# Performance work log

Measured on AMD Instinct MI355X. Metric: run time of the kernel, lower is better.

## Reference

```python
import jax, jax.numpy as jnp
import numpy as np

N_NODES = 50000
N_EDGES = 800000
NODE_F = 5
EDGE_F = 4
HID = 128


def _glorot(key, shape):
    fan_in, fan_out = shape[0], shape[1]
    lim = float(np.sqrt(6.0 / (fan_in + fan_out)))
    return jax.random.uniform(key, shape, jnp.float32, -lim, lim)


def setup_inputs() -> dict:
    key = jax.random.key(0)
    ks = jax.random.split(key, 12)
    x = jax.random.normal(ks[0], (N_NODES, NODE_F), jnp.float32)
    edge_attr = jax.random.normal(ks[1], (N_EDGES, EDGE_F), jnp.float32)
    edge_index = jax.random.randint(ks[2], (2, N_EDGES), 0, N_NODES, jnp.int64)
    return {
        "x": x,
        "edge_attr": edge_attr,
        "W1": _glorot(ks[3], (NODE_F, HID)),
        "b1": jnp.zeros((HID,), jnp.float32),
        "W2": _glorot(ks[4], (HID, HID)),
        "b2": jnp.zeros((HID,), jnp.float32),
        "Wm1": _glorot(ks[5], (2 * HID + EDGE_F, HID)),
        "bm1": jnp.zeros((HID,), jnp.float32),
        "Wm2": _glorot(ks[6], (HID, 1)),
        "bm2": jnp.zeros((1,), jnp.float32),
        "edge_index": edge_index,
    }


def _gcn_conv(x, W, b, row, col, norm, n_nodes):
    # GCNConv: out = D^{-1/2} (A + I) D^{-1/2} X W + b
    xw = x @ W                                   # [N, H]
    msg = norm[:, None] * xw[row]                # [E+N, H] gather + scale
    agg = jax.ops.segment_sum(msg, col, num_segments=n_nodes)
    return agg + b


def reference(x, edge_attr, W1, b1, W2, b2, Wm1, bm1, Wm2, bm2, edge_index):
    n = x.shape[0]
    src, dst = edge_index[0], edge_index[1]
    # add self-loops (PyG GCNConv default)
    loop = jnp.arange(n, dtype=edge_index.dtype)
    row = jnp.concatenate([src, loop])
    col = jnp.concatenate([dst, loop])
    # symmetric normalization, in-degree w/ self-loops
    deg = jax.ops.segment_sum(jnp.ones_like(col, dtype=x.dtype), col, num_segments=n)
    dis = jnp.where(deg > 0, jax.lax.rsqrt(deg), 0.0)
    norm = dis[row] * dis[col]

    h = jax.nn.relu(_gcn_conv(x, W1, b1, row, col, norm, n))
    h = _gcn_conv(h, W2, b2, row, col, norm, n)

    # gather-concat edge MLP
    edge_emb = jnp.concatenate([h[src], h[dst], edge_attr], axis=1)  # [E, 2H+F]
    out = jax.nn.relu(edge_emb @ Wm1 + bm1) @ Wm2 + bm2              # [E, 1]
    return jax.nn.sigmoid(out[:, 0])
```

## Files before the change

### kernel.cpp

```cpp
#include <hip/hip_runtime.h>
#include <math.h>

#define HID 128
typedef unsigned int uint;
typedef __attribute__((ext_vector_type(8))) __bf16 bf16x8;
typedef __attribute__((ext_vector_type(4))) float f32x4;
typedef __attribute__((ext_vector_type(2))) float f32x2;


__device__ __forceinline__ uint pack_bf2(float x, float y) {
    union { float f; uint u; } a, b;
    a.f = x; b.f = y;
    uint lo = (a.u + 0x7fffu + ((a.u >> 16) & 1u)) >> 16;
    uint hi = (b.u + 0x7fffu + ((b.u >> 16) & 1u)) & 0xffff0000u;
    return lo | hi;
}

__device__ __forceinline__ unsigned short bf16r(float x) {
    union { float f; uint u; } a; a.f = x;
    return (unsigned short)((a.u + 0x7fffu + ((a.u >> 16) & 1u)) >> 16);
}

__device__ __forceinline__ f32x2 bf2f(uint v) {
    union { uint u[2]; f32x2 f; } r;
    r.u[0] = v << 16;
    r.u[1] = v & 0xffff0000u;
    return r.f;
}

__device__ __forceinline__ f32x2 mk2(float s) { f32x2 r; r.x = s; r.y = s; return r; }
__device__ __forceinline__ f32x2 max2z(f32x2 a) {
    f32x2 r; r.x = fmaxf(a.x, 0.f); r.y = fmaxf(a.y, 0.f); return r;
}
__device__ __forceinline__ f32x2 shfl_xor2(f32x2 v, int m) {
    f32x2 r; r.x = __shfl_xor(v.x, m, 64); r.y = __shfl_xor(v.y, m, 64); return r;
}


__global__ void prep_kernel(const float* __restrict__ W2, const float* __restrict__ Wm1,
                            const float* __restrict__ b2, const float* __restrict__ bm1,
                            uint* __restrict__ fWc, float* __restrict__ brow) {
    int t0 = blockIdx.x * blockDim.x + threadIdx.x;
    if (t0 < 16384) {
        int i = t0;
        int p = i & 3, lane = (i >> 2) & 63, kk = (i >> 8) & 3, ct = i >> 10;
        int k = kk * 32 + (lane >> 4) * 8 + p * 2;
        int n2 = ct * 16 + (lane & 15);
        const float* wmc = (n2 < 128) ? (Wm1 + n2) : (Wm1 + 128 * HID + (n2 - 128));
        const float* w2r0 = W2 + (size_t)k * HID;
        const float* w2r1 = w2r0 + HID;
        float d0 = 0.f, d1 = 0.f;
        for (int j = 0; j < HID; ++j) {
            float wm = wmc[(size_t)j * HID];
            d0 += w2r0[j] * wm;
            d1 += w2r1[j] * wm;
        }
        fWc[i] = pack_bf2(d0, d1);
    } else if (t0 < 16384 + 256) {
        int i = t0 - 16384;
        const float* wmc = (i < 128) ? (Wm1 + i) : (Wm1 + 128 * HID + (i - 128));
        float d = 0.f;
        for (int j = 0; j < HID; ++j) d += b2[j] * wmc[(size_t)j * HID];
        brow[i] = d + ((i < 128) ? bm1[i] : 0.f);
    }
}

__global__ void hist_rank(const int* __restrict__ dst, int* __restrict__ cnt,
                          int* __restrict__ rank, int E) {
    int e = blockIdx.x * blockDim.x + threadIdx.x;
    if (e < E) rank[e] = atomicAdd(&cnt[dst[e]], 1);
}

__global__ void scan1(const int* __restrict__ cnt, int* __restrict__ excl,
                      int* __restrict__ bsum, int N) {
    __shared__ int sh[256];
    int tid = threadIdx.x;
    int gid = blockIdx.x * 256 + tid;
    int v = (gid < N) ? cnt[gid] : 0;
    sh[tid] = v;
    __syncthreads();
    for (int o = 1; o < 256; o <<= 1) {
        int t = (tid >= o) ? sh[tid - o] : 0;
        __syncthreads();
        sh[tid] += t;
        __syncthreads();
    }
    if (gid < N) excl[gid] = sh[tid] - v;
    if (tid == 255) bsum[blockIdx.x] = sh[255];
}

__global__ void scan3x(const int* __restrict__ cnt, int* __restrict__ rowptr,
                       const int* __restrict__ bsum,
                       float* __restrict__ dis, const float* __restrict__ x,
                       uint4* __restrict__ xps, int N, int E, int NB) {
    __shared__ int sh[256];
    __shared__ int ex[256];
    int tid = threadIdx.x;
    int v = (tid < NB) ? bsum[tid] : 0;
    sh[tid] = v;
    __syncthreads();
    for (int o = 1; o < 256; o <<= 1) {
        int t = (tid >= o) ? sh[tid - o] : 0;
        __syncthreads();
        sh[tid] += t;
        __syncthreads();
    }
    ex[tid] = sh[tid] - v;
    __syncthreads();
    int gid = blockIdx.x * 256 + tid;
    if (gid < N) {
        rowptr[gid] = rowptr[gid] + ex[blockIdx.x];
        float dn = rsqrtf((float)cnt[gid] + 1.0f);
        dis[gid] = dn;
        const float* xr = x + (size_t)gid * 5;
        uint4 pk;
        pk.x = pack_bf2(dn * xr[0], dn * xr[1]);
        pk.y = pack_bf2(dn * xr[2], dn * xr[3]);
        pk.z = pack_bf2(dn * xr[4], 0.f);
        pk.w = 0u;
        xps[gid] = pk;
    }
    if (gid == N) rowptr[N] = E;
}

__global__ void scatter2(const int* __restrict__ src, const int* __restrict__ dst,
                         const int* __restrict__ rowptr, const int* __restrict__ rank,
                         uint2* __restrict__ csr2, int E) {
    int e = blockIdx.x * blockDim.x + threadIdx.x;
    if (e < E) {
        int d = dst[e];
        int pos = rowptr[d] + rank[e];
        csr2[pos] = make_uint2((uint)src[e] | ((uint)d << 16), (uint)e);
    }
}

__launch_bounds__(256)
__global__ void layer1_kernel(const uint4* __restrict__ xps, const uint2* __restrict__ csr2,
                              const int* __restrict__ rowptr, const float* __restrict__ dis,
                              const float* __restrict__ W1, const float* __restrict__ b1,
                              uint* __restrict__ hs1, int N) {
    __shared__ float sW[5 * HID];
    __shared__ float sb[HID];
    int tid = threadIdx.x;
    for (int i = tid; i < 5 * HID; i += 256) sW[i] = W1[i];
    for (int i = tid; i < HID; i += 256) sb[i] = b1[i];
    __syncthreads();

    int n = blockIdx.x * 256 + tid;
    if (n >= N) return;
    int beg = rowptr[n], end = rowptr[n + 1];
    float a0 = 0.f, a1 = 0.f, a2 = 0.f, a3 = 0.f, a4 = 0.f;
    for (int i = beg; i < end; ++i) {
        int s = (int)(csr2[i].x & 0xffffu);
        uint4 v = xps[s];
        f32x2 v01 = bf2f(v.x), v23 = bf2f(v.y), v4 = bf2f(v.z);
        a0 += v01.x; a1 += v01.y; a2 += v23.x; a3 += v23.y; a4 += v4.x;
    }
    {
        uint4 v = xps[n];
        f32x2 v01 = bf2f(v.x), v23 = bf2f(v.y), v4 = bf2f(v.z);
        a0 += v01.x; a1 += v01.y; a2 += v23.x; a3 += v23.y; a4 += v4.x;
    }
    float dn = dis[n];
    a0 *= dn; a1 *= dn; a2 *= dn; a3 *= dn; a4 *= dn;

    uint* op = hs1 + (size_t)n * 64;
    #pragma unroll 4
    for (int p = 0; p < 64; ++p) {
        int j = p * 2;
        float t0 = sb[j]     + a0 * sW[j]     + a1 * sW[HID + j]     + a2 * sW[2*HID + j]
                             + a3 * sW[3*HID + j] + a4 * sW[4*HID + j];
        float t1 = sb[j + 1] + a0 * sW[j + 1] + a1 * sW[HID + j + 1] + a2 * sW[2*HID + j + 1]
                             + a3 * sW[3*HID + j + 1] + a4 * sW[4*HID + j + 1];
        op[p] = pack_bf2(fmaxf(t0, 0.f) * dn, fmaxf(t1, 0.f) * dn);
    }
}

__launch_bounds__(256)
__global__ void agg_gemm(const uint4* __restrict__ hs1, const uint2* __restrict__ csr2,
                         const int* __restrict__ rowptr, const float* __restrict__ dis,
                         const uint4* __restrict__ Bf, const float* __restrict__ brow,
                         unsigned short* __restrict__ out, int N) {
    __shared__ uint gt[16][64];
    int wave = threadIdx.x >> 6, lane = threadIdx.x & 63;
    int gl = lane & 15, grp = lane >> 4;
    int nb = blockIdx.x * 16;

    for (int q = 0; q < 4; ++q) {
        int r = wave * 4 + q;
        int n = nb + r;
        if (n < N) {
            int beg = rowptr[n], end = rowptr[n + 1];
            f32x2 acc[4];
            #pragma unroll
            for (int p = 0; p < 4; ++p) acc[p] = mk2(0.f);
            for (int base = beg + grp; base < end; base += 16) {
                int i1 = base + 4, i2 = base + 8, i3 = base + 12;
                int s0 = (int)(csr2[base].x & 0xffffu);
                int s1 = (int)(csr2[(i1 < end) ? i1 : beg].x & 0xffffu);
                int s2 = (int)(csr2[(i2 < end) ? i2 : beg].x & 0xffffu);
                int s3 = (int)(csr2[(i3 < end) ? i3 : beg].x & 0xffffu);
                uint4 v0 = hs1[(size_t)s0 * 16 + gl];
                uint4 v1 = hs1[(size_t)s1 * 16 + gl];
                uint4 v2 = hs1[(size_t)s2 * 16 + gl];
                uint4 v3 = hs1[(size_t)s3 * 16 + gl];
                f32x2 w1 = mk2((i1 < end) ? 1.f : 0.f);
                f32x2 w2 = mk2((i2 < end) ? 1.f : 0.f);
                f32x2 w3 = mk2((i3 < end) ? 1.f : 0.f);
                acc[0] += bf2f(v0.x);  acc[1] += bf2f(v0.y);
                acc[2] += bf2f(v0.z);  acc[3] += bf2f(v0.w);
                acc[0] += bf2f(v1.x) * w1;  acc[1] += bf2f(v1.y) * w1;
                acc[2] += bf2f(v1.z) * w1;  acc[3] += bf2f(v1.w) * w1;
                acc[0] += bf2f(v2.x) * w2;  acc[1] += bf2f(v2.y) * w2;
                acc[2] += bf2f(v2.z) * w2;  acc[3] += bf2f(v2.w) * w2;
                acc[0] += bf2f(v3.x) * w3;  acc[1] += bf2f(v3.y) * w3;
                acc[2] += bf2f(v3.z) * w3;  acc[3] += bf2f(v3.w) * w3;
            }
            #pragma unroll
            for (int p = 0; p < 4; ++p) {
                acc[p] += shfl_xor2(acc[p], 16);
                acc[p] += shfl_xor2(acc[p], 32);
            }
            if (grp == 0) {
                uint4 sv = hs1[(size_t)n * 16 + gl];
                f32x2 dn = mk2(dis[n]);
                f32x2 o0 = (acc[0] + bf2f(sv.x)) * dn;
                f32x2 o1 = (acc[1] + bf2f(sv.y)) * dn;
                f32x2 o2 = (acc[2] + bf2f(sv.z)) * dn;
                f32x2 o3 = (acc[3] + bf2f(sv.w)) * dn;
                gt[r][gl * 4]     = pack_bf2(o0.x, o0.y);
                gt[r][gl * 4 + 1] = pack_bf2(o1.x, o1.y);
                gt[r][gl * 4 + 2] = pack_bf2(o2.x, o2.y);
                gt[r][gl * 4 + 3] = pack_bf2(o3.x, o3.y);
            }
        } else if (grp == 0) {
            gt[r][gl * 4] = 0; gt[r][gl * 4 + 1] = 0;
            gt[r][gl * 4 + 2] = 0; gt[r][gl * 4 + 3] = 0;
        }
    }
    __syncthreads();

    int quad = lane >> 4;
    bf16x8 afr[4];
    #pragma unroll
    for (int kk = 0; kk < 4; ++kk)
        afr[kk] = *(const bf16x8*)&gt[gl][kk * 16 + quad * 4];

    for (int cc = 0; cc < 4; ++cc) {
        int c = wave * 4 + cc;
        f32x4 acc = {0.f, 0.f, 0.f, 0.f};
        #pragma unroll
        for (int kk = 0; kk < 4; ++kk) {
            bf16x8 bfr = *(const bf16x8*)&Bf[(size_t)(c * 4 + kk) * 64 + lane];
            acc = __builtin_amdgcn_mfma_f32_16x16x32_bf16(afr[kk], bfr, acc, 0, 0, 0);
        }
        float bv = brow[c * 16 + gl];
        #pragma unroll
        for (int reg = 0; reg < 4; ++reg) {
            int row = nb + quad * 4 + reg;
            if (row < N)
                out[(size_t)row * 256 + c * 16 + gl] = bf16r(acc[reg] + bv);
        }
    }
}

__launch_bounds__(256)
__global__ void edge_mlp_kernel(const uint4* __restrict__ HsHd, const float4* __restrict__ ea,
                                const uint2* __restrict__ csr2,
                                const float* __restrict__ Wb, const float* __restrict__ Wm2,
                                const float* __restrict__ bm2,
                                float* __restrict__ out, int E) {
    int lane = threadIdx.x & 63;
    int gl = lane & 15, grp = lane >> 4;

    f32x2 wb[4][4], w2[4];
    #pragma unroll
    for (int k = 0; k < 4; ++k) {
        const f32x2* wp = (const f32x2*)(Wb + k * HID + gl * 8);
        #pragma unroll
        for (int p = 0; p < 4; ++p) wb[k][p] = wp[p];
    }
    {
        const f32x2* wp = (const f32x2*)(Wm2 + gl * 8);
        #pragma unroll
        for (int p = 0; p < 4; ++p) w2[p] = wp[p];
    }
    float b2v = bm2[0];

    int gwave = (blockIdx.x * blockDim.x + threadIdx.x) >> 6;
    int nw = (gridDim.x * blockDim.x) >> 6;
    for (int base = gwave * 16; base < E; base += nw * 16) {
        int i0 = base + grp * 4;
        uint2 ce[4];
        uint4 hv[4], dv[4];
        float4 eav[4];
        #pragma unroll
        for (int t = 0; t < 4; ++t) {
            int i = i0 + t;
            int j = (i < E) ? i : (E - 1);
            ce[t] = csr2[j];
            hv[t] = HsHd[(size_t)(ce[t].x & 0xffffu) * 32 + gl];
            dv[t] = HsHd[(size_t)(ce[t].x >> 16) * 32 + 16 + gl];
            eav[t] = ea[ce[t].y];
        }
        float pr[4];
        #pragma unroll
        for (int t = 0; t < 4; ++t) {
            uint hu[4] = {hv[t].x, hv[t].y, hv[t].z, hv[t].w};
            uint du[4] = {dv[t].x, dv[t].y, dv[t].z, dv[t].w};
            f32x2 e0 = mk2(eav[t].x), e1 = mk2(eav[t].y);
            f32x2 e2 = mk2(eav[t].z), e3 = mk2(eav[t].w);
            f32x2 p2 = mk2(0.f);
            #pragma unroll
            for (int p = 0; p < 4; ++p) {
                f32x2 tt = bf2f(hu[p]) + bf2f(du[p]);
                tt += e0 * wb[0][p];
                tt += e1 * wb[1][p];
                tt += e2 * wb[2][p];
                tt += e3 * wb[3][p];
                tt = max2z(tt);
                p2 += tt * w2[p];
            }
            pr[t] = p2.x + p2.y;
        }
        #pragma unroll
        for (int o = 1; o <= 8; o <<= 1) {
            #pragma unroll
            for (int t = 0; t < 4; ++t) pr[t] += __shfl_xor(pr[t], o, 64);
        }
        if (gl == 0) {
            #pragma unroll
            for (int t = 0; t < 4; ++t) {
                int i = i0 + t;
                if (i < E)
                    out[ce[t].y] = 1.f / (1.f + exp2f(-1.44269504f * (pr[t] + b2v)));
            }
        }
    }
}


extern "C" void kernel_launch(void* const* d_in, const int* in_sizes, int n_in,
                              void* d_out, int out_size, void* d_ws, size_t ws_size,
                              hipStream_t stream) {
    const float* x    = (const float*)d_in[0];
    const float* ea   = (const float*)d_in[1];
    const float* W1   = (const float*)d_in[2];
    const float* b1   = (const float*)d_in[3];
    const float* W2   = (const float*)d_in[4];
    const float* b2   = (const float*)d_in[5];
    const float* Wm1  = (const float*)d_in[6];
    const float* bm1  = (const float*)d_in[7];
    const float* Wm2  = (const float*)d_in[8];
    const float* bm2  = (const float*)d_in[9];
    const int*   ei   = (const int*)d_in[10];

    const int N = in_sizes[0] / 5;
    const int E = in_sizes[1] / 4;
    const int* src = ei;
    const int* dst = ei + E;
    float* out = (float*)d_out;

    char* ws = (char*)d_ws;
    size_t off = 0;
    auto alloc = [&](size_t bytes) -> void* {
        void* p = ws + off;
        off = (off + bytes + 255) & ~(size_t)255;
        return p;
    };
    int*    cnt    = (int*)alloc((size_t)N * 4);
    int*    rowptr = (int*)alloc((size_t)(N + 1) * 4);
    int*    bsum   = (int*)alloc(256 * 4);
    float*  dis    = (float*)alloc((size_t)N * 4);
    int*    rank   = (int*)alloc((size_t)(E + 8) * 4);
    uint2*  csr2   = (uint2*)alloc((size_t)(E + 8) * 8);
    uint4*  xps    = (uint4*)alloc((size_t)N * 16);
    uint*   hs1    = (uint*)alloc((size_t)N * 64 * 4);
    uint*   HsHd   = (uint*)alloc((size_t)N * 128 * 4);
    uint*   fWc    = (uint*)alloc(16384 * 4);
    float*  brow   = (float*)alloc(256 * 4);
    (void)ws_size; (void)n_in; (void)out_size;

    const int NB = (N + 255) / 256;
    const int EB = (E + 255) / 256;

    hipMemsetAsync(cnt, 0, (size_t)N * 4, stream);
    prep_kernel<<<65, 256, 0, stream>>>(W2, Wm1, b2, bm1, fWc, brow);
    hist_rank<<<EB, 256, 0, stream>>>(dst, cnt, rank, E);
    scan1<<<NB, 256, 0, stream>>>(cnt, rowptr, bsum, N);
    scan3x<<<NB, 256, 0, stream>>>(cnt, rowptr, bsum, dis, x, xps, N, E, NB);
    scatter2<<<EB, 256, 0, stream>>>(src, dst, rowptr, rank, csr2, E);

    layer1_kernel<<<NB, 256, 0, stream>>>(xps, csr2, rowptr, dis, W1, b1, hs1, N);

    agg_gemm<<<(N + 15) / 16, 256, 0, stream>>>((const uint4*)hs1, csr2, rowptr, dis,
                                                (const uint4*)fWc, brow,
                                                (unsigned short*)HsHd, N);

    edge_mlp_kernel<<<2048, 256, 0, stream>>>((const uint4*)HsHd, (const float4*)ea, csr2,
                                              Wm1 + 256 * HID, Wm2, bm2, out, E);
}
```

Measured before the change: 264.1 us.

## Split reductions across lanes with DPP and prefetch CSR entries in edge MLP

The prep kernel splits each 128-long dot product over 4 lanes and combines the partials with DPP adds, using four times as many threads. layer1 assigns 4 threads per node, splitting both the neighbour gather and the output columns. agg_gemm preloads a wave's rowptr values once, and indexing is changed to 32-bit. The edge MLP prefetches the next iteration's CSR entries and replaces the shuffle reductions with DPP row operations. The aim is more parallelism and less latency in small serial kernels, at the cost of extra threads and reliance on DPP row semantics being correct.

```diff
diff --git a/kernel.cpp b/kernel.cpp
--- a/kernel.cpp
+++ b/kernel.cpp
@@ -32,8 +32,13 @@
 __device__ __forceinline__ f32x2 max2z(f32x2 a) {
     f32x2 r; r.x = fmaxf(a.x, 0.f); r.y = fmaxf(a.y, 0.f); return r;
 }
-__device__ __forceinline__ f32x2 shfl_xor2(f32x2 v, int m) {
-    f32x2 r; r.x = __shfl_xor(v.x, m, 64); r.y = __shfl_xor(v.y, m, 64); return r;
+
+template<int CTRL>
+__device__ __forceinline__ float dpp_add(float x) {
+    union { float f; int i; } u, r;
+    u.f = x;
+    r.i = __builtin_amdgcn_update_dpp(0, u.i, CTRL, 0xf, 0xf, true);
+    return x + r.f;
 }
 
 
@@ -41,27 +46,35 @@
                             const float* __restrict__ b2, const float* __restrict__ bm1,
                             uint* __restrict__ fWc, float* __restrict__ brow) {
     int t0 = blockIdx.x * blockDim.x + threadIdx.x;
-    if (t0 < 16384) {
-        int i = t0;
+    if (t0 < 65536) {
+        int ks = t0 & 3;
+        int i = t0 >> 2;
         int p = i & 3, lane = (i >> 2) & 63, kk = (i >> 8) & 3, ct = i >> 10;
         int k = kk * 32 + (lane >> 4) * 8 + p * 2;
         int n2 = ct * 16 + (lane & 15);
         const float* wmc = (n2 < 128) ? (Wm1 + n2) : (Wm1 + 128 * HID + (n2 - 128));
-        const float* w2r0 = W2 + (size_t)k * HID;
+        const float* w2r0 = W2 + (size_t)k * HID + ks * 32;
         const float* w2r1 = w2r0 + HID;
+        const float* wm = wmc + (size_t)(ks * 32) * HID;
         float d0 = 0.f, d1 = 0.f;
-        for (int j = 0; j < HID; ++j) {
-            float wm = wmc[(size_t)j * HID];
-            d0 += w2r0[j] * wm;
-            d1 += w2r1[j] * wm;
-        }
-        fWc[i] = pack_bf2(d0, d1);
-    } else if (t0 < 16384 + 256) {
-        int i = t0 - 16384;
+        #pragma unroll 8
+        for (int j = 0; j < 32; ++j) {
+            float w = wm[(size_t)j * HID];
+            d0 += w2r0[j] * w;
+            d1 += w2r1[j] * w;
+        }
+        d0 = dpp_add<0xB1>(d0); d0 = dpp_add<0x4E>(d0);
+        d1 = dpp_add<0xB1>(d1); d1 = dpp_add<0x4E>(d1);
+        if (ks == 0) fWc[i] = pack_bf2(d0, d1);
+    } else if (t0 < 65536 + 1024) {
+        int r = t0 - 65536;
+        int ks = r & 3;
+        int i = r >> 2;
         const float* wmc = (i < 128) ? (Wm1 + i) : (Wm1 + 128 * HID + (i - 128));
         float d = 0.f;
-        for (int j = 0; j < HID; ++j) d += b2[j] * wmc[(size_t)j * HID];
-        brow[i] = d + ((i < 128) ? bm1[i] : 0.f);
+        for (int j = ks * 32; j < ks * 32 + 32; ++j) d += b2[j] * wmc[(size_t)j * HID];
+        d = dpp_add<0xB1>(d); d = dpp_add<0x4E>(d);
+        if (ks == 0) brow[i] = d + ((i < 128) ? bm1[i] : 0.f);
     }
 }
 
@@ -146,16 +159,22 @@
     for (int i = tid; i < HID; i += 256) sb[i] = b1[i];
     __syncthreads();
 
-    int n = blockIdx.x * 256 + tid;
+    int sub = tid & 3;
+    int n = blockIdx.x * 64 + (tid >> 2);
     if (n >= N) return;
     int beg = rowptr[n], end = rowptr[n + 1];
     float a0 = 0.f, a1 = 0.f, a2 = 0.f, a3 = 0.f, a4 = 0.f;
-    for (int i = beg; i < end; ++i) {
-        int s = (int)(csr2[i].x & 0xffffu);
+    for (int i = beg + sub; i < end; i += 4) {
+        uint s = csr2[i].x & 0xffffu;
         uint4 v = xps[s];
         f32x2 v01 = bf2f(v.x), v23 = bf2f(v.y), v4 = bf2f(v.z);
         a0 += v01.x; a1 += v01.y; a2 += v23.x; a3 += v23.y; a4 += v4.x;
     }
+    a0 = dpp_add<0xB1>(a0); a0 = dpp_add<0x4E>(a0);
+    a1 = dpp_add<0xB1>(a1); a1 = dpp_add<0x4E>(a1);
+    a2 = dpp_add<0xB1>(a2); a2 = dpp_add<0x4E>(a2);
+    a3 = dpp_add<0xB1>(a3); a3 = dpp_add<0x4E>(a3);
+    a4 = dpp_add<0xB1>(a4); a4 = dpp_add<0x4E>(a4);
     {
         uint4 v = xps[n];
         f32x2 v01 = bf2f(v.x), v23 = bf2f(v.y), v4 = bf2f(v.z);
@@ -165,14 +184,15 @@
     a0 *= dn; a1 *= dn; a2 *= dn; a3 *= dn; a4 *= dn;
 
     uint* op = hs1 + (size_t)n * 64;
-    #pragma unroll 4
-    for (int p = 0; p < 64; ++p) {
-        int j = p * 2;
+    #pragma unroll
+    for (int p = 0; p < 16; ++p) {
+        int q = p * 4 + sub;
+        int j = q * 2;
         float t0 = sb[j]     + a0 * sW[j]     + a1 * sW[HID + j]     + a2 * sW[2*HID + j]
                              + a3 * sW[3*HID + j] + a4 * sW[4*HID + j];
         float t1 = sb[j + 1] + a0 * sW[j + 1] + a1 * sW[HID + j + 1] + a2 * sW[2*HID + j + 1]
                              + a3 * sW[3*HID + j + 1] + a4 * sW[4*HID + j + 1];
-        op[p] = pack_bf2(fmaxf(t0, 0.f) * dn, fmaxf(t1, 0.f) * dn);
+        op[q] = pack_bf2(fmaxf(t0, 0.f) * dn, fmaxf(t1, 0.f) * dn);
     }
 }
 
@@ -185,25 +205,33 @@
     int wave = threadIdx.x >> 6, lane = threadIdx.x & 63;
     int gl = lane & 15, grp = lane >> 4;
     int nb = blockIdx.x * 16;
+    int r0 = nb + wave * 4;
+
+    int rp[5];
+    #pragma unroll
+    for (int j = 0; j < 5; ++j) {
+        int idx = r0 + j;
+        rp[j] = rowptr[(idx <= N) ? idx : N];
+    }
 
     for (int q = 0; q < 4; ++q) {
         int r = wave * 4 + q;
         int n = nb + r;
         if (n < N) {
-            int beg = rowptr[n], end = rowptr[n + 1];
+            int beg = rp[q], end = rp[q + 1];
             f32x2 acc[4];
             #pragma unroll
             for (int p = 0; p < 4; ++p) acc[p] = mk2(0.f);
             for (int base = beg + grp; base < end; base += 16) {
                 int i1 = base + 4, i2 = base + 8, i3 = base + 12;
-                int s0 = (int)(csr2[base].x & 0xffffu);
-                int s1 = (int)(csr2[(i1 < end) ? i1 : beg].x & 0xffffu);
-                int s2 = (int)(csr2[(i2 < end) ? i2 : beg].x & 0xffffu);
-                int s3 = (int)(csr2[(i3 < end) ? i3 : beg].x & 0xffffu);
-                uint4 v0 = hs1[(size_t)s0 * 16 + gl];
-                uint4 v1 = hs1[(size_t)s1 * 16 + gl];
-                uint4 v2 = hs1[(size_t)s2 * 16 + gl];
-                uint4 v3 = hs1[(size_t)s3 * 16 + gl];
+                uint s0 = csr2[base].x & 0xffffu;
+                uint s1 = csr2[(i1 < end) ? i1 : beg].x & 0xffffu;
+                uint s2 = csr2[(i2 < end) ? i2 : beg].x & 0xffffu;
+                uint s3 = csr2[(i3 < end) ? i3 : beg].x & 0xffffu;
+                uint4 v0 = hs1[(s0 << 4) + (uint)gl];
+                uint4 v1 = hs1[(s1 << 4) + (uint)gl];
+                uint4 v2 = hs1[(s2 << 4) + (uint)gl];
+                uint4 v3 = hs1[(s3 << 4) + (uint)gl];
                 f32x2 w1 = mk2((i1 < end) ? 1.f : 0.f);
                 f32x2 w2 = mk2((i2 < end) ? 1.f : 0.f);
                 f32x2 w3 = mk2((i3 < end) ? 1.f : 0.f);
@@ -218,11 +246,14 @@
             }
             #pragma unroll
             for (int p = 0; p < 4; ++p) {
-                acc[p] += shfl_xor2(acc[p], 16);
-                acc[p] += shfl_xor2(acc[p], 32);
+                f32x2 t;
+                t.x = __shfl_xor(acc[p].x, 16, 64); t.y = __shfl_xor(acc[p].y, 16, 64);
+                acc[p] += t;
+                t.x = __shfl_xor(acc[p].x, 32, 64); t.y = __shfl_xor(acc[p].y, 32, 64);
+                acc[p] += t;
             }
             if (grp == 0) {
-                uint4 sv = hs1[(size_t)n * 16 + gl];
+                uint4 sv = hs1[((uint)n << 4) + (uint)gl];
                 f32x2 dn = mk2(dis[n]);
                 f32x2 o0 = (acc[0] + bf2f(sv.x)) * dn;
                 f32x2 o1 = (acc[1] + bf2f(sv.y)) * dn;
@@ -289,20 +320,40 @@
 
     int gwave = (blockIdx.x * blockDim.x + threadIdx.x) >> 6;
     int nw = (gridDim.x * blockDim.x) >> 6;
-    for (int base = gwave * 16; base < E; base += nw * 16) {
-        int i0 = base + grp * 4;
-        uint2 ce[4];
+    int stride = nw * 16;
+    int base = gwave * 16;
+    if (base >= E) return;
+
+    uint2 ce[4];
+    #pragma unroll
+    for (int t = 0; t < 4; ++t) {
+        int i = base + grp * 4 + t;
+        ce[t] = csr2[(i < E) ? i : 0];
+    }
+
+    while (base < E) {
+        int nbase = base + stride;
+
         uint4 hv[4], dv[4];
         float4 eav[4];
+        uint eid[4];
         #pragma unroll
         for (int t = 0; t < 4; ++t) {
-            int i = i0 + t;
-            int j = (i < E) ? i : (E - 1);
-            ce[t] = csr2[j];
-            hv[t] = HsHd[(size_t)(ce[t].x & 0xffffu) * 32 + gl];
-            dv[t] = HsHd[(size_t)(ce[t].x >> 16) * 32 + 16 + gl];
-            eav[t] = ea[ce[t].y];
-        }
+            uint cx = ce[t].x;
+            eid[t] = ce[t].y;
+            hv[t] = HsHd[((cx & 0xffffu) << 5) + (uint)gl];
+            dv[t] = HsHd[((cx >> 16) << 5) + 16u + (uint)gl];
+            eav[t] = ea[eid[t]];
+        }
+
+        if (nbase < E) {
+            #pragma unroll
+            for (int t = 0; t < 4; ++t) {
+                int i = nbase + grp * 4 + t;
+                ce[t] = csr2[(i < E) ? i : 0];
+            }
+        }
+
         float pr[4];
         #pragma unroll
         for (int t = 0; t < 4; ++t) {
@@ -324,18 +375,23 @@
             pr[t] = p2.x + p2.y;
         }
         #pragma unroll
-        for (int o = 1; o <= 8; o <<= 1) {
-            #pragma unroll
-            for (int t = 0; t < 4; ++t) pr[t] += __shfl_xor(pr[t], o, 64);
+        for (int t = 0; t < 4; ++t) {
+            float s = pr[t];
+            s = dpp_add<0xB1>(s);
+            s = dpp_add<0x4E>(s);
+            s = dpp_add<0x124>(s);
+            s = dpp_add<0x128>(s);
+            pr[t] = s;
         }
         if (gl == 0) {
             #pragma unroll
             for (int t = 0; t < 4; ++t) {
-                int i = i0 + t;
+                int i = base + grp * 4 + t;
                 if (i < E)
-                    out[ce[t].y] = 1.f / (1.f + exp2f(-1.44269504f * (pr[t] + b2v)));
-            }
-        }
+                    out[eid[t]] = 1.f / (1.f + exp2f(-1.44269504f * (pr[t] + b2v)));
+            }
+        }
+        base = nbase;
     }
 }
 
@@ -385,13 +441,13 @@
     const int EB = (E + 255) / 256;
 
     hipMemsetAsync(cnt, 0, (size_t)N * 4, stream);
-    prep_kernel<<<65, 256, 0, stream>>>(W2, Wm1, b2, bm1, fWc, brow);
+    prep_kernel<<<260, 256, 0, stream>>>(W2, Wm1, b2, bm1, fWc, brow);
     hist_rank<<<EB, 256, 0, stream>>>(dst, cnt, rank, E);
     scan1<<<NB, 256, 0, stream>>>(cnt, rowptr, bsum, N);
     scan3x<<<NB, 256, 0, stream>>>(cnt, rowptr, bsum, dis, x, xps, N, E, NB);
     scatter2<<<EB, 256, 0, stream>>>(src, dst, rowptr, rank, csr2, E);
 
-    layer1_kernel<<<NB, 256, 0, stream>>>(xps, csr2, rowptr, dis, W1, b1, hs1, N);
+    layer1_kernel<<<(N + 63) / 64, 256, 0, stream>>>(xps, csr2, rowptr, dis, W1, b1, hs1, N);
 
     agg_gemm<<<(N + 15) / 16, 256, 0, stream>>>((const uint4*)hs1, csr2, rowptr, dis,
                                                 (const uint4*)fWc, brow,
```

New measurement: 252.5 us. -4.4%, faster.
